# Kernel tuning notes

Measured on AMD Instinct MI355X. Metric: run time of the kernel, lower is better.

The kernel has to match this reference:

```python
import jax, jax.numpy as jnp
import numpy as np

# dims: batch, tokens, model dim, heads, head_dim, context len, n_blocks, ffn dim
B, L, D, H, HD, S, NB, DFF = 1, 3072, 1024, 16, 64, 512, 2, 4096
T3, H3, W3 = 12, 16, 16  # latent video grid, T3*H3*W3 == L


def _ln(x):
    # LayerNorm, elementwise_affine=False, eps=1e-6
    m = jnp.mean(x, axis=-1, keepdims=True)
    v = jnp.mean(jnp.square(x - m), axis=-1, keepdims=True)
    return (x - m) * jax.lax.rsqrt(v + 1e-6)


def _rot_half(x):
    x1, x2 = jnp.split(x, 2, axis=-1)
    return jnp.concatenate([-x2, x1], axis=-1)


def _rope3d(head_dim, t, h, w):
    d = head_dim // 6
    def band(n):
        freqs = 1.0 / 10000.0 ** (np.arange(0, 2 * d, 2, dtype=np.float32) / (2 * d))
        return np.outer(np.arange(n, dtype=np.float32), freqs)  # [n, d]
    te, he, we = band(t), band(h), band(w)
    rope = np.zeros((t, h, w, head_dim), dtype=np.float32)
    rope[:, :, :, :d] = te[:, None, None, :]
    rope[:, :, :, d:2 * d] = he[None, :, None, :]
    rope[:, :, :, 2 * d:3 * d] = we[None, None, :, :]
    return jnp.asarray(rope.reshape(t * h * w, head_dim))


def _forward(x, timestep_emb, context_emb, rope_emb, adaW, adab, sqW, skW, svW,
             soW, sob, cqW, ckW, cvW, coW, cob, f1W, f1b, f2W, f2b):
    Bv, Lv, Dv = x.shape
    hd = rope_emb.shape[-1]
    nh = Dv // hd
    scale = hd ** -0.5
    cos = jnp.cos(rope_emb)[None, None]  # [1,1,L,hd]
    sin = jnp.sin(rope_emb)[None, None]

    def heads(y):  # [B,N,D] -> [B,H,N,hd]
        return y.reshape(Bv, -1, nh, hd).transpose(0, 2, 1, 3)

    def merge(y):  # [B,H,L,hd] -> [B,L,D]
        return y.transpose(0, 2, 1, 3).reshape(Bv, Lv, Dv)

    for i in range(adaW.shape[0]):
        mods = timestep_emb @ adaW[i].T + adab[i]  # [B, 6D]
        sh_msa, sc_msa, g_msa, sh_mlp, sc_mlp, g_mlp = jnp.split(mods, 6, axis=-1)
        # --- AdaLN + self-attention with RoPE ---
        hx = _ln(x) * (1.0 + sc_msa[:, None, :]) + sh_msa[:, None, :]
        q, k, v = heads(hx @ sqW[i].T), heads(hx @ skW[i].T), heads(hx @ svW[i].T)
        q = q * cos + _rot_half(q) * sin
        k = k * cos + _rot_half(k) * sin
        a = jax.nn.softmax(jnp.einsum('bhld,bhmd->bhlm', q, k) * scale, axis=-1)
        o = merge(jnp.einsum('bhlm,bhmd->bhld', a, v))
        x = x + g_msa[:, None, :] * (o @ soW[i].T + sob[i])
        # --- cross-attention (no gate, no modulation) ---
        hx = _ln(x)
        q = heads(hx @ cqW[i].T)
        k = heads(context_emb @ ckW[i].T)
        v = heads(context_emb @ cvW[i].T)
        a = jax.nn.softmax(jnp.einsum('bhld,bhsd->bhls', q, k) * scale, axis=-1)
        o = merge(jnp.einsum('bhls,bhsd->bhld', a, v))
        x = x + (o @ coW[i].T + cob[i])
        # --- AdaLN + MLP (exact GELU) ---
        hx = _ln(x) * (1.0 + sc_mlp[:, None, :]) + sh_mlp[:, None, :]
        hx = jax.nn.gelu(hx @ f1W[i].T + f1b[i], approximate=False)
        x = x + g_mlp[:, None, :] * (hx @ f2W[i].T + f2b[i])
    return x


def setup_inputs() -> dict:
    ks = jax.random.split(jax.random.key(0), 20)
    s = 0.02
    return {
        'x': jax.random.normal(ks[0], (B, L, D), jnp.float32),
        'timestep_emb': jax.random.normal(ks[1], (B, D), jnp.float32),
        'context_emb': jax.random.normal(ks[2], (B, S, D), jnp.float32),
        'rope_emb': _rope3d(HD, T3, H3, W3),
        'adaW': jax.random.normal(ks[3], (NB, 6 * D, D), jnp.float32) * s,
        'adab': jnp.zeros((NB, 6 * D), jnp.float32),
        'sqW': jax.random.normal(ks[4], (NB, D, D), jnp.float32) * s,
        'skW': jax.random.normal(ks[5], (NB, D, D), jnp.float32) * s,
        'svW': jax.random.normal(ks[6], (NB, D, D), jnp.float32) * s,
        'soW': jax.random.normal(ks[7], (NB, D, D), jnp.float32) * s,
        'sob': jnp.zeros((NB, D), jnp.float32),
        'cqW': jax.random.normal(ks[8], (NB, D, D), jnp.float32) * s,
        'ckW': jax.random.normal(ks[9], (NB, D, D), jnp.float32) * s,
        'cvW': jax.random.normal(ks[10], (NB, D, D), jnp.float32) * s,
        'coW': jax.random.normal(ks[11], (NB, D, D), jnp.float32) * s,
        'cob': jnp.zeros((NB, D), jnp.float32),
        'f1W': jax.random.normal(ks[12], (NB, DFF, D), jnp.float32) * s,
        'f1b': jnp.zeros((NB, DFF), jnp.float32),
        'f2W': jax.random.normal(ks[13], (NB, D, DFF), jnp.float32) * s,
        'f2b': jnp.zeros((NB, D), jnp.float32),
    }


def reference(x, timestep_emb, context_emb, rope_emb, adaW, adab, sqW, skW, svW,
              soW, sob, cqW, ckW, cvW, coW, cob, f1W, f1b, f2W, f2b):
    return _forward(x, timestep_emb, context_emb, rope_emb, adaW, adab, sqW, skW,
                    svW, soW, sob, cqW, ckW, cvW, coW, cob, f1W, f1b, f2W, f2b)
```

## Files before the change

### kernel.cpp

```cpp
#include <hip/hip_runtime.h>
#include <math.h>

typedef __attribute__((ext_vector_type(8))) short bf16x8;
typedef __attribute__((ext_vector_type(4))) float f32x4;
typedef unsigned short u16;
typedef unsigned int u32;

#define DEV static __device__ __forceinline__

typedef __attribute__((address_space(3))) u32 lds_u32;
typedef const __attribute__((address_space(1))) u32 glb_u32;

DEV void gload16(const void* g, void* l){
  __builtin_amdgcn_global_load_lds((glb_u32*)g, (lds_u32*)l, 16, 0, 0);
}

DEV u16 f2bf(float f){
  u32 u = __builtin_bit_cast(u32, f);
  u32 r = (u + 0x7fffu + ((u >> 16) & 1u)) >> 16;
  return (u16)r;
}
DEV float bf2f(u16 h){
  u32 u = ((u32)h) << 16;
  return __builtin_bit_cast(float, u);
}
DEV u32 cvtpk(float a, float b){
  u32 r;
  asm("v_cvt_pk_bf16_f32 %0, %1, %2" : "=v"(r) : "v"(a), "v"(b));
  return r;
}
DEV float gelu_exact(float x){ return 0.5f*x*(1.f+erff(x*0.70710678118654752f)); }

#define QSCALE 0.18033688f

DEV void xcd_remap(int &bx, int &by){
  int gx = gridDim.x, gy = gridDim.y;
  int n = gx*gy;
  if ((n & 7) == 0){
    int id = by*gx + bx;
    int q = n >> 3;
    int sid = (id & 7)*q + (id >> 3);
    bx = sid % gx;
    by = sid / gx;
  }
}

__global__ __launch_bounds__(256) void k_copy_f32(const float* __restrict__ in, float* __restrict__ out, int n4){
  int i = blockIdx.x*256 + threadIdx.x;
  if (i < n4) ((float4*)out)[i] = ((const float4*)in)[i];
}

__global__ __launch_bounds__(256) void k_cvt_bf16(const float* __restrict__ in, u16* __restrict__ out, int n4){
  int i = blockIdx.x*256 + threadIdx.x;
  if (i < n4){
    float4 v = ((const float4*)in)[i];
    ushort4 o;
    o.x = f2bf(v.x); o.y = f2bf(v.y); o.z = f2bf(v.z); o.w = f2bf(v.w);
    ((ushort4*)out)[i] = o;
  }
}

struct CvtArgs { const float4* s[16]; ushort4* d[16]; };
__global__ __launch_bounds__(256) void k_cvt_all(CvtArgs a){
  int i = blockIdx.x*256 + threadIdx.x;
  int seg = i >> 19;
  int off = i & 0x7FFFF;
  float4 v = a.s[seg][off];
  ushort4 o;
  o.x = f2bf(v.x); o.y = f2bf(v.y); o.z = f2bf(v.z); o.w = f2bf(v.w);
  a.d[seg][off] = o;
}

__global__ __launch_bounds__(256) void k_trig(const float* __restrict__ rope,
    float2* __restrict__ ctq, float2* __restrict__ ctk){
  int i = blockIdx.x*256 + threadIdx.x;
  int d = i & 63;
  float a = rope[i];
  float c = cosf(a), s = sinf(a);
  float sg = (d < 32) ? -s : s;
  ctk[i] = make_float2(c, sg);
  ctq[i] = make_float2(c*QSCALE, sg*QSCALE);
}

__global__ __launch_bounds__(256) void k_ada(const float* __restrict__ te,
    const float* __restrict__ adaW, const float* __restrict__ adab,
    float* __restrict__ mods){
  int row = blockIdx.x*4 + (threadIdx.x>>6);
  int lane = threadIdx.x & 63;
  const float* wr = adaW + (size_t)row*1024;
  float s = 0.f;
  #pragma unroll
  for (int j=0; j<4; j++){
    int c = lane*4 + j*256;
    float4 a = *(const float4*)(te + c);
    float4 b = *(const float4*)(wr + c);
    s += a.x*b.x + a.y*b.y + a.z*b.z + a.w*b.w;
  }
  #pragma unroll
  for (int off=32; off; off>>=1) s += __shfl_down(s, off);
  if (!lane) mods[row] = s + adab[row];
}

__global__ __launch_bounds__(256) void k_ln_mod(const float* __restrict__ x,
    const float* __restrict__ sh, const float* __restrict__ sc,
    u16* __restrict__ out){
  int row = blockIdx.x, t = threadIdx.x;
  const float* xr = x + (size_t)row*1024;
  float4 v = ((const float4*)xr)[t];
  float s  = v.x+v.y+v.z+v.w;
  float sq = v.x*v.x+v.y*v.y+v.z*v.z+v.w*v.w;
  #pragma unroll
  for (int off=32; off; off>>=1){ s += __shfl_down(s,off); sq += __shfl_down(sq,off); }
  __shared__ float red[8];
  int w = t>>6, lane = t&63;
  if (!lane){ red[w] = s; red[4+w] = sq; }
  __syncthreads();
  s  = red[0]+red[1]+red[2]+red[3];
  sq = red[4]+red[5]+red[6]+red[7];
  float mean = s*(1.f/1024.f);
  float var  = sq*(1.f/1024.f) - mean*mean;
  float rst  = rsqrtf(var + 1e-6f);
  float vv[4] = {v.x, v.y, v.z, v.w};
  ushort4 o;
  u16 ob[4];
  #pragma unroll
  for (int j=0;j<4;j++){
    int col = t*4+j;
    float y = (vv[j]-mean)*rst;
    if (sh) y = y*(1.f + sc[col]) + sh[col];
    ob[j] = f2bf(y);
  }
  o.x=ob[0]; o.y=ob[1]; o.z=ob[2]; o.w=ob[3];
  *(ushort4*)(out + (size_t)row*1024 + t*4) = o;
}

__global__ __launch_bounds__(256) void k_rope(u16* __restrict__ q, u16* __restrict__ k,
    const float* __restrict__ rope){
  int idx = blockIdx.x*256 + threadIdx.x;
  int d = idx & 31;
  int h = (idx >> 5) & 15;
  int p = idx >> 9;
  const float* rr = rope + (size_t)p*64;
  float a0 = rr[d], a1 = rr[d+32];
  float c0 = cosf(a0), s0 = sinf(a0);
  float c1 = cosf(a1), s1 = sinf(a1);
  size_t o = (size_t)p*1024 + h*64 + d;
  float q0 = bf2f(q[o]), q1 = bf2f(q[o+32]);
  q[o]    = f2bf((q0*c0 - q1*s0)*QSCALE);
  q[o+32] = f2bf((q1*c1 + q0*s1)*QSCALE);
  float k0 = bf2f(k[o]), k1 = bf2f(k[o+32]);
  k[o]    = f2bf(k0*c0 - k1*s0);
  k[o+32] = f2bf(k1*c1 + k0*s1);
}

DEV void gemm_loop(const u16* __restrict__ X, const u16* __restrict__ W,
                   int bm, int bn, int ld, int lenK, u16* As, u16* Bs, f32x4 acc[4][4])
{
  int t = threadIdx.x;
  int w = t>>6, lane = t&63;
  int wr = (w>>1)*64, wc = (w&1)*64;
  int fr = lane&15, g = lane>>4;
  int arow = lane>>2, acol = (lane&3)*8;
  const u16* xp = X + (size_t)(bm + w*32 + arow)*ld + acol;
  const u16* wp = W + (size_t)(bn + w*32 + arow)*ld + acol;
  int nk = lenK >> 5;
  {
    u16* a = As + w*1024; u16* b = Bs + w*1024;
    gload16(xp, a);             gload16(xp + (size_t)16*ld, a + 512);
    gload16(wp, b);             gload16(wp + (size_t)16*ld, b + 512);
  }
  for (int kt = 0; kt < nk; ++kt){
    __syncthreads();
    int cur = kt & 1;
    if (kt + 1 < nk){
      int nb = cur ^ 1;
      int k0 = (kt+1) << 5;
      u16* a = As + nb*4096 + w*1024; u16* b = Bs + nb*4096 + w*1024;
      gload16(xp + k0, a);        gload16(xp + k0 + (size_t)16*ld, a + 512);
      gload16(wp + k0, b);        gload16(wp + k0 + (size_t)16*ld, b + 512);
    }
    const u16* ab = As + cur*4096;
    const u16* bb = Bs + cur*4096;
    bf16x8 a[4], b[4];
    #pragma unroll
    for (int i=0;i<4;i++) a[i] = *(const bf16x8*)(ab + (wr+i*16+fr)*32 + g*8);
    #pragma unroll
    for (int i=0;i<4;i++) b[i] = *(const bf16x8*)(bb + (wc+i*16+fr)*32 + g*8);
    __builtin_amdgcn_s_setprio(1);
    #pragma unroll
    for (int i=0;i<4;i++)
      #pragma unroll
      for (int j=0;j<4;j++)
        acc[i][j] = __builtin_amdgcn_mfma_f32_16x16x32_bf16(a[i], b[j], acc[i][j], 0, 0, 0);
    __builtin_amdgcn_s_setprio(0);
  }
}

template<int EPI>
__global__ __launch_bounds__(256) void k_gemm_bf16(
    const u16* __restrict__ X, const u16* __restrict__ W,
    const float* __restrict__ bias,
    u16* __restrict__ Yout,
    const float* __restrict__ resin, float* __restrict__ resout,
    const float* __restrict__ gate,
    int M, int N, int K)
{
  __shared__ __align__(16) u16 As[2*128*32];
  __shared__ __align__(16) u16 Bs[2*128*32];
  int bx = blockIdx.x, by = blockIdx.y;
  xcd_remap(bx, by);
  int bm = bx*128, bn = by*128;
  f32x4 acc[4][4] = {};
  gemm_loop(X, W, bm, bn, K, K, As, Bs, acc);
  int lane = threadIdx.x & 63, w = threadIdx.x>>6;
  int wr = (w>>1)*64, wc = (w&1)*64;
  int fr = lane&15, g = lane>>4;
  #pragma unroll
  for (int i=0;i<4;i++){
    #pragma unroll
    for (int j=0;j<4;j++){
      int col = bn + wc + j*16 + fr;
      float bv = bias ? bias[col] : 0.f;
      #pragma unroll
      for (int r=0;r<4;r++){
        int row = bm + wr + i*16 + g*4 + r;
        float y = acc[i][j][r] + bv;
        if (EPI == 1){
          Yout[(size_t)row*N + col] = f2bf(gelu_exact(y));
        } else if (EPI == 2){
          float gt = gate ? gate[col] : 1.f;
          resout[(size_t)row*N + col] = resin[(size_t)row*N + col] + gt*y;
        } else {
          Yout[(size_t)row*N + col] = f2bf(y*QSCALE);
        }
      }
    }
  }
}

__global__ __launch_bounds__(256) void k_gemm_part(
    const u16* __restrict__ X, const u16* __restrict__ W,
    float* __restrict__ pp, int M, int N, int K, int Ks)
{
  __shared__ __align__(16) u16 As[2*128*32];
  __shared__ __align__(16) u16 Bs[2*128*32];
  int bx = blockIdx.x, by = blockIdx.y;
  xcd_remap(bx, by);
  int s = blockIdx.z;
  int bm = bx*128, bn = by*128;
  f32x4 acc[4][4] = {};
  gemm_loop(X + (size_t)s*Ks, W + (size_t)s*Ks, bm, bn, K, Ks, As, Bs, acc);
  float* out = pp + (size_t)s*M*N;
  int lane = threadIdx.x & 63, w = threadIdx.x>>6;
  int wr = (w>>1)*64, wc = (w&1)*64;
  int fr = lane&15, g = lane>>4;
  #pragma unroll
  for (int i=0;i<4;i++)
    #pragma unroll
    for (int j=0;j<4;j++){
      int col = bn + wc + j*16 + fr;
      #pragma unroll
      for (int r=0;r<4;r++){
        int row = bm + wr + i*16 + g*4 + r;
        out[(size_t)row*N + col] = acc[i][j][r];
      }
    }
}

template<int EPI>
__global__ __launch_bounds__(256) void k_reduce(
    const float* __restrict__ pp, int S, const float* __restrict__ bias,
    const float* __restrict__ resin, float* __restrict__ resout,
    const float* __restrict__ gate, u16* __restrict__ Ybf,
    int MN, int N)
{
  int idx = blockIdx.x*256 + threadIdx.x;
  int base = idx*4;
  if (base >= MN) return;
  float4 s4 = *(const float4*)(pp + base);
  for (int s=1; s<S; ++s){
    float4 t4 = *(const float4*)(pp + (size_t)s*MN + base);
    s4.x += t4.x; s4.y += t4.y; s4.z += t4.z; s4.w += t4.w;
  }
  int col = base & (N-1);
  float b0=0,b1=0,b2=0,b3=0;
  if (bias){ b0=bias[col]; b1=bias[col+1]; b2=bias[col+2]; b3=bias[col+3]; }
  if (EPI == 2){
    float g0=1,g1=1,g2=1,g3=1;
    if (gate){ g0=gate[col]; g1=gate[col+1]; g2=gate[col+2]; g3=gate[col+3]; }
    float4 rv = *(const float4*)(resin + base);
    float4 o;
    o.x = rv.x + g0*(s4.x+b0);
    o.y = rv.y + g1*(s4.y+b1);
    o.z = rv.z + g2*(s4.z+b2);
    o.w = rv.w + g3*(s4.w+b3);
    *(float4*)(resout + base) = o;
  } else {
    ushort4 o;
    o.x = f2bf((s4.x+b0)*QSCALE);
    o.y = f2bf((s4.y+b1)*QSCALE);
    o.z = f2bf((s4.z+b2)*QSCALE);
    o.w = f2bf((s4.w+b3)*QSCALE);
    *(ushort4*)(Ybf + base) = o;
  }
}

template<int MOD>
__global__ __launch_bounds__(256) void k_reduce_ln(
    const float* __restrict__ pp, int S, const float* __restrict__ bias,
    const float* __restrict__ resin, float* __restrict__ resout,
    const float* __restrict__ gate,
    const float* __restrict__ sh, const float* __restrict__ sc,
    u16* __restrict__ hx)
{
  int row = blockIdx.x, t = threadIdx.x;
  size_t base = (size_t)row*1024 + t*4;
  const size_t MN = (size_t)3072*1024;
  float4 s4 = *(const float4*)(pp + base);
  for (int s=1; s<S; ++s){
    float4 t4 = *(const float4*)(pp + (size_t)s*MN + base);
    s4.x += t4.x; s4.y += t4.y; s4.z += t4.z; s4.w += t4.w;
  }
  int col = t*4;
  float b0=0,b1=0,b2=0,b3=0;
  if (bias){ b0=bias[col]; b1=bias[col+1]; b2=bias[col+2]; b3=bias[col+3]; }
  float g0=1,g1=1,g2=1,g3=1;
  if (gate){ g0=gate[col]; g1=gate[col+1]; g2=gate[col+2]; g3=gate[col+3]; }
  float4 rv = *(const float4*)(resin + base);
  float y[4];
  y[0] = rv.x + g0*(s4.x+b0);
  y[1] = rv.y + g1*(s4.y+b1);
  y[2] = rv.z + g2*(s4.z+b2);
  y[3] = rv.w + g3*(s4.w+b3);
  float4 ov; ov.x=y[0]; ov.y=y[1]; ov.z=y[2]; ov.w=y[3];
  *(float4*)(resout + base) = ov;
  float s  = y[0]+y[1]+y[2]+y[3];
  float sq = y[0]*y[0]+y[1]*y[1]+y[2]*y[2]+y[3]*y[3];
  #pragma unroll
  for (int off=32; off; off>>=1){ s += __shfl_down(s,off); sq += __shfl_down(sq,off); }
  __shared__ float red[8];
  int w = t>>6, lane = t&63;
  if (!lane){ red[w] = s; red[4+w] = sq; }
  __syncthreads();
  s  = red[0]+red[1]+red[2]+red[3];
  sq = red[4]+red[5]+red[6]+red[7];
  float mean = s*(1.f/1024.f);
  float var  = sq*(1.f/1024.f) - mean*mean;
  float rst  = rsqrtf(var + 1e-6f);
  ushort4 o;
  u16 ob[4];
  #pragma unroll
  for (int j=0;j<4;j++){
    float yy = (y[j]-mean)*rst;
    if (MOD) yy = yy*(1.f + sc[col+j]) + sh[col+j];
    ob[j] = f2bf(yy);
  }
  o.x=ob[0]; o.y=ob[1]; o.z=ob[2]; o.w=ob[3];
  *(ushort4*)(hx + base) = o;
}

template<int MODE>
__global__ __launch_bounds__(256) void k_qkv(
    const u16* __restrict__ X,
    const u16* __restrict__ W0, const u16* __restrict__ W1, const u16* __restrict__ W2,
    u16* __restrict__ Y0, u16* __restrict__ Y1, u16* __restrict__ VT,
    const float2* __restrict__ ctq, const float2* __restrict__ ctk,
    int M, int ldvt)
{
  __shared__ __align__(16) u16 As[2*128*32];
  __shared__ __align__(16) u16 Bs[2*128*32];
  int bx = blockIdx.x, by = blockIdx.y;
  xcd_remap(bx, by);
  int bm = bx*128, bn = by*128;
  int sel = bn >> 10;
  int bnl = bn & 1023;
  const u16* W = (sel==0 ? W0 : (sel==1 ? W1 : W2));
  f32x4 acc[4][4] = {};
  gemm_loop(X, W, bm, bnl, 1024, 1024, As, Bs, acc);
  int lane = threadIdx.x & 63, w = threadIdx.x>>6;
  int wr = (w>>1)*64, wc = (w&1)*64;
  int fr = lane&15, g = lane>>4;
  if (sel < 2){
    u16* Y = (sel==0) ? Y0 : Y1;
    const float2* ct = (sel==0) ? ctq : ctk;
    #pragma unroll
    for (int i=0;i<4;i++)
      #pragma unroll
      for (int j=0;j<4;j++){
        int col = bnl + wc + j*16 + fr;
        int d = j*16 + fr;
        #pragma unroll
        for (int r=0;r<4;r++){
          int row = bm + wr + i*16 + g*4 + r;
          float2 cs = ct[row*64 + d];
          float yv = acc[i][j][r]*cs.x + acc[i][j^2][r]*cs.y;
          Y[(size_t)row*1024 + col] = f2bf(yv);
        }
      }
  } else {
    #pragma unroll
    for (int i=0;i<4;i++)
      #pragma unroll
      for (int j=0;j<4;j++){
        int col = bnl + wc + j*16 + fr;
        int row0 = bm + wr + i*16 + g*4;
        uint2 pk;
        pk.x = cvtpk(acc[i][j][0], acc[i][j][1]);
        pk.y = cvtpk(acc[i][j][2], acc[i][j][3]);
        *(uint2*)(VT + (size_t)col*ldvt + row0) = pk;
      }
  }
}

__global__ __launch_bounds__(256) void k_kv64(
    const u16* __restrict__ X,
    const u16* __restrict__ Wk, const u16* __restrict__ Wv,
    u16* __restrict__ Kout, u16* __restrict__ VTout, int ldvt)
{
  __shared__ __align__(16) u16 As[2*64*32];
  __shared__ __align__(16) u16 Bs[2*64*32];
  int bx = blockIdx.x, by = blockIdx.y;
  xcd_remap(bx, by);
  int bm = bx*64;
  int sel = by >> 4;
  int bnl = (by & 15)*64;
  const u16* W = sel ? Wv : Wk;
  int t = threadIdx.x, w = t>>6, lane = t&63;
  int wr = (w>>1)*32, wc = (w&1)*32;
  int fr = lane&15, g = lane>>4;
  f32x4 acc[2][2] = {};
  int arow = lane>>2, acol = (lane&3)*8;
  const u16* xp = X + (size_t)(bm + w*16 + arow)*1024 + acol;
  const u16* wp = W + (size_t)(bnl + w*16 + arow)*1024 + acol;
  {
    gload16(xp, As + w*512);
    gload16(wp, Bs + w*512);
  }
  for (int kt = 0; kt < 32; ++kt){
    __syncthreads();
    int cur = kt & 1;
    if (kt + 1 < 32){
      int nb = cur ^ 1;
      int k0 = (kt+1) << 5;
      gload16(xp + k0, As + nb*2048 + w*512);
      gload16(wp + k0, Bs + nb*2048 + w*512);
    }
    const u16* ab = As + cur*2048;
    const u16* bb = Bs + cur*2048;
    bf16x8 a[2], b[2];
    #pragma unroll
    for (int i=0;i<2;i++) a[i] = *(const bf16x8*)(ab + (wr+i*16+fr)*32 + g*8);
    #pragma unroll
    for (int i=0;i<2;i++) b[i] = *(const bf16x8*)(bb + (wc+i*16+fr)*32 + g*8);
    __builtin_amdgcn_s_setprio(1);
    #pragma unroll
    for (int i=0;i<2;i++)
      #pragma unroll
      for (int j=0;j<2;j++)
        acc[i][j] = __builtin_amdgcn_mfma_f32_16x16x32_bf16(a[i], b[j], acc[i][j], 0, 0, 0);
    __builtin_amdgcn_s_setprio(0);
  }
  #pragma unroll
  for (int i=0;i<2;i++)
    #pragma unroll
    for (int j=0;j<2;j++){
      int col = bnl + wc + j*16 + fr;
      if (sel == 0){
        #pragma unroll
        for (int r=0;r<4;r++){
          int row = bm + wr + i*16 + g*4 + r;
          Kout[(size_t)row*1024 + col] = f2bf(acc[i][j][r]);
        }
      } else {
        int row0 = bm + wr + i*16 + g*4;
        uint2 pk;
        pk.x = cvtpk(acc[i][j][0], acc[i][j][1]);
        pk.y = cvtpk(acc[i][j][2], acc[i][j][3]);
        *(uint2*)(VTout + (size_t)col*ldvt + row0) = pk;
      }
    }
}

template<int EPI>
__global__ __launch_bounds__(256) void k_gemm_f32(
    const u16* __restrict__ X, const float* __restrict__ W,
    const float* __restrict__ bias,
    u16* __restrict__ Yout,
    const float* __restrict__ resin, float* __restrict__ resout,
    const float* __restrict__ gate,
    int M, int N, int K)
{
  __shared__ __align__(16) u16 As[128][32];
  __shared__ __align__(16) u16 Bs[128][40];
  int bx = blockIdx.x, by = blockIdx.y;
  xcd_remap(bx, by);
  int bm = bx*128, bn = by*128;
  int t = threadIdx.x;
  int w = t>>6, lane = t&63;
  int wr = (w>>1)*64, wc = (w&1)*64;
  int fr = lane&15, g = lane>>4;
  f32x4 acc[4][4] = {};
  int arow = lane>>2, acol = (lane&3)*8;
  int srow = t>>2, scol = (t&3)*8;
  for (int k0=0; k0<K; k0+=32){
    #pragma unroll
    for (int inst=0; inst<2; ++inst){
      int r = w*32 + inst*16 + arow;
      gload16(X + (size_t)(bm+r)*K + k0 + acol, &As[w*32+inst*16][0]);
    }
    #pragma unroll
    for (int it=0; it<2; ++it){
      const float* wp = W + (size_t)(bn+srow+it*64)*K + k0 + scol;
      float4 f0 = *(const float4*)(wp);
      float4 f1 = *(const float4*)(wp+4);
      uint4 bw;
      bw.x = (u32)f2bf(f0.x) | ((u32)f2bf(f0.y)<<16);
      bw.y = (u32)f2bf(f0.z) | ((u32)f2bf(f0.w)<<16);
      bw.z = (u32)f2bf(f1.x) | ((u32)f2bf(f1.y)<<16);
      bw.w = (u32)f2bf(f1.z) | ((u32)f2bf(f1.w)<<16);
      *(uint4*)&Bs[srow+it*64][scol] = bw;
    }
    __syncthreads();
    bf16x8 a[4], b[4];
    #pragma unroll
    for (int i=0;i<4;i++) a[i] = *(const bf16x8*)&As[wr+i*16+fr][g*8];
    #pragma unroll
    for (int i=0;i<4;i++) b[i] = *(const bf16x8*)&Bs[wc+i*16+fr][g*8];
    #pragma unroll
    for (int i=0;i<4;i++)
      #pragma unroll
      for (int j=0;j<4;j++)
        acc[i][j] = __builtin_amdgcn_mfma_f32_16x16x32_bf16(a[i], b[j], acc[i][j], 0, 0, 0);
    __syncthreads();
  }
  #pragma unroll
  for (int i=0;i<4;i++){
    #pragma unroll
    for (int j=0;j<4;j++){
      int col = bn + wc + j*16 + fr;
      float bv = bias ? bias[col] : 0.f;
      #pragma unroll
      for (int r=0;r<4;r++){
        int row = bm + wr + i*16 + g*4 + r;
        float y = acc[i][j][r] + bv;
        if (EPI == 0){
          Yout[(size_t)row*N + col] = f2bf(y);
        } else if (EPI == 1){
          Yout[(size_t)row*N + col] = f2bf(gelu_exact(y));
        } else if (EPI == 2){
          float gt = gate ? gate[col] : 1.f;
          resout[(size_t)row*N + col] = resin[(size_t)row*N + col] + gt*y;
        } else if (EPI == 3){
          Yout[(size_t)col*M + row] = f2bf(y);
        } else {
          Yout[(size_t)row*N + col] = f2bf(y*QSCALE);
        }
      }
    }
  }
}

__global__ __launch_bounds__(128) void k_flash(
    const u16* __restrict__ Q, const u16* __restrict__ Kb, const u16* __restrict__ VT,
    u16* __restrict__ O, int Lkv)
{
  __shared__ __align__(16) u16 Ks[2*64*64];
  __shared__ __align__(16) u16 Vs[2*64*64];
  __shared__ __align__(16) u16 Ps[2][32][72];
  int bx = blockIdx.x, by = blockIdx.y;
  xcd_remap(bx, by);
  int h = by;
  int q0 = bx*64;
  int t = threadIdx.x, w = t>>6, lane = t&63;
  int fr = lane&15, g = lane>>4;
  bf16x8 aq0[2], aq1[2];
  #pragma unroll
  for (int qg=0; qg<2; ++qg){
    const u16* qrow = Q + (size_t)(q0 + w*32 + qg*16 + fr)*1024 + h*64;
    aq0[qg] = *(const bf16x8*)(qrow + g*8);
    aq1[qg] = *(const bf16x8*)(qrow + 32 + g*8);
  }
  f32x4 accO[2][4] = {};
  float l0 = 0.f, l1 = 0.f;
  int slot = lane & 7, rop = lane >> 3;
  const u16* kbase = Kb + (size_t)h*64;
  const u16* vbase = VT + (size_t)h*64*Lkv;
  int nt = Lkv >> 6;
  auto stage = [&](int tt, int buf){
    int k0 = tt << 6;
    #pragma unroll
    for (int ps=0; ps<4; ++ps){
      int row = ps*16 + w*8 + rop;
      int ss = slot ^ (row & 7);
      gload16(kbase + (size_t)(k0+row)*1024 + ss*8, Ks + buf*4096 + row*64);
      gload16(vbase + (size_t)row*Lkv + k0 + ss*8, Vs + buf*4096 + row*64);
    }
  };
  stage(0, 0);
  for (int tt=0; tt<nt; ++tt){
    __syncthreads();
    int cur = tt & 1;
    if (tt+1 < nt) stage(tt+1, cur^1);
    const u16* kc = Ks + cur*4096;
    const u16* vc = Vs + cur*4096;
    f32x4 st0[4] = {}, st1[4] = {};
    __builtin_amdgcn_s_setprio(1);
    #pragma unroll
    for (int kb=0;kb<4;kb++){
      int rowK = kb*16 + fr;
      bf16x8 kA0 = *(const bf16x8*)(kc + rowK*64 + ((g  ) ^ (rowK&7))*8);
      bf16x8 kA1 = *(const bf16x8*)(kc + rowK*64 + ((4+g) ^ (rowK&7))*8);
      st0[kb] = __builtin_amdgcn_mfma_f32_16x16x32_bf16(kA0, aq0[0], st0[kb], 0,0,0);
      st0[kb] = __builtin_amdgcn_mfma_f32_16x16x32_bf16(kA1, aq1[0], st0[kb], 0,0,0);
      st1[kb] = __builtin_amdgcn_mfma_f32_16x16x32_bf16(kA0, aq0[1], st1[kb], 0,0,0);
      st1[kb] = __builtin_amdgcn_mfma_f32_16x16x32_bf16(kA1, aq1[1], st1[kb], 0,0,0);
    }
    __builtin_amdgcn_s_setprio(0);
    {
      float ts = 0.f;
      u32 pk[8];
      #pragma unroll
      for (int kb=0;kb<4;kb++){
        float p0 = exp2f(st0[kb][0]);
        float p1 = exp2f(st0[kb][1]);
        float p2 = exp2f(st0[kb][2]);
        float p3 = exp2f(st0[kb][3]);
        ts += (p0+p1)+(p2+p3);
        pk[kb*2]   = cvtpk(p0,p1);
        pk[kb*2+1] = cvtpk(p2,p3);
      }
      ts += __shfl_xor(ts, 16);
      ts += __shfl_xor(ts, 32);
      l0 += ts;
      #pragma unroll
      for (int kb=0;kb<4;kb++){
        uint2 pv; pv.x = pk[kb*2]; pv.y = pk[kb*2+1];
        *(uint2*)&Ps[w][fr][kb*16 + g*4] = pv;
      }
    }
    {
      float ts = 0.f;
      u32 pk[8];
      #pragma unroll
      for (int kb=0;kb<4;kb++){
        float p0 = exp2f(st1[kb][0]);
        float p1 = exp2f(st1[kb][1]);
        float p2 = exp2f(st1[kb][2]);
        float p3 = exp2f(st1[kb][3]);
        ts += (p0+p1)+(p2+p3);
        pk[kb*2]   = cvtpk(p0,p1);
        pk[kb*2+1] = cvtpk(p2,p3);
      }
      ts += __shfl_xor(ts, 16);
      ts += __shfl_xor(ts, 32);
      l1 += ts;
      #pragma unroll
      for (int kb=0;kb<4;kb++){
        uint2 pv; pv.x = pk[kb*2]; pv.y = pk[kb*2+1];
        *(uint2*)&Ps[w][16+fr][kb*16 + g*4] = pv;
      }
    }
    bf16x8 ap0g0 = *(const bf16x8*)&Ps[w][fr][g*8];
    bf16x8 ap1g0 = *(const bf16x8*)&Ps[w][fr][32 + g*8];
    bf16x8 ap0g1 = *(const bf16x8*)&Ps[w][16+fr][g*8];
    bf16x8 ap1g1 = *(const bf16x8*)&Ps[w][16+fr][32 + g*8];
    __builtin_amdgcn_s_setprio(1);
    #pragma unroll
    for (int nd=0; nd<4; nd++){
      int rowV = nd*16 + fr;
      bf16x8 vB0 = *(const bf16x8*)(vc + rowV*64 + ((g  ) ^ (rowV&7))*8);
      bf16x8 vB1 = *(const bf16x8*)(vc + rowV*64 + ((4+g) ^ (rowV&7))*8);
      accO[0][nd] = __builtin_amdgcn_mfma_f32_16x16x32_bf16(ap0g0, vB0, accO[0][nd], 0,0,0);
      accO[0][nd] = __builtin_amdgcn_mfma_f32_16x16x32_bf16(ap1g0, vB1, accO[0][nd], 0,0,0);
      accO[1][nd] = __builtin_amdgcn_mfma_f32_16x16x32_bf16(ap0g1, vB0, accO[1][nd], 0,0,0);
      accO[1][nd] = __builtin_amdgcn_mfma_f32_16x16x32_bf16(ap1g1, vB1, accO[1][nd], 0,0,0);
    }
    __builtin_amdgcn_s_setprio(0);
  }
  #pragma unroll
  for (int qg=0; qg<2; ++qg){
    float rl = 1.f / (qg ? l1 : l0);
    #pragma unroll
    for (int r=0;r<4;r++){
      float rlq = __shfl(rl, g*4+r);
      int row = q0 + w*32 + qg*16 + g*4 + r;
      #pragma unroll
      for (int nd=0; nd<4; nd++)
        O[(size_t)row*1024 + h*64 + nd*16 + fr] = f2bf(accO[qg][nd][r] * rlq);
    }
  }
}

extern "C" void kernel_launch(void* const* d_in, const int* in_sizes, int n_in,
                              void* d_out, int out_size, void* d_ws, size_t ws_size,
                              hipStream_t stream){
  const float* x_in = (const float*)d_in[0];
  const float* te   = (const float*)d_in[1];
  const float* ctx  = (const float*)d_in[2];
  const float* rope = (const float*)d_in[3];
  const float* adaW = (const float*)d_in[4];
  const float* adab = (const float*)d_in[5];
  const float* sqW  = (const float*)d_in[6];
  const float* skW  = (const float*)d_in[7];
  const float* svW  = (const float*)d_in[8];
  const float* soW  = (const float*)d_in[9];
  const float* sob  = (const float*)d_in[10];
  const float* cqW  = (const float*)d_in[11];
  const float* ckW  = (const float*)d_in[12];
  const float* cvW  = (const float*)d_in[13];
  const float* coW  = (const float*)d_in[14];
  const float* cob  = (const float*)d_in[15];
  const float* f1W  = (const float*)d_in[16];
  const float* f1b  = (const float*)d_in[17];
  const float* f2W  = (const float*)d_in[18];
  const float* f2b  = (const float*)d_in[19];
  float* x = (float*)d_out;

  char* p = (char*)d_ws;
  size_t used = 0;
  auto alloc = [&](size_t bytes){
    void* r = (void*)(p + used);
    used += (bytes + 255) & ~(size_t)255;
    return r;
  };
  u16* hx   = (u16*)alloc((size_t)3072*1024*2);
  u16* qb   = (u16*)alloc((size_t)3072*1024*2);
  u16* kb   = (u16*)alloc((size_t)3072*1024*2);
  u16* vt   = (u16*)alloc((size_t)1024*3072*2);
  u16* ob   = (u16*)alloc((size_t)3072*1024*2);
  u16* mid  = (u16*)alloc((size_t)3072*4096*2);
  u16* ctxb = (u16*)alloc((size_t)512*1024*2);
  float* mods = (float*)alloc((size_t)2*6144*4);
  float2* ctq = (float2*)alloc((size_t)3072*64*8);
  float2* ctk = (float2*)alloc((size_t)3072*64*8);
  size_t base_used = used;
  const size_t NW_SMALL = (size_t)2*1024*1024;
  const size_t NW_BIG   = (size_t)2*4096*1024;
  size_t wbytes = (8*NW_SMALL + 2*NW_BIG)*2;
  bool pre = (base_used + wbytes + 4096) <= ws_size;

  u16 *sqWb=nullptr,*skWb=nullptr,*svWb=nullptr,*soWb=nullptr,
      *cqWb=nullptr,*ckWb=nullptr,*cvWb=nullptr,*coWb=nullptr,
      *f1Wb=nullptr,*f2Wb=nullptr;
  if (pre){
    sqWb=(u16*)alloc(NW_SMALL*2); skWb=(u16*)alloc(NW_SMALL*2);
    svWb=(u16*)alloc(NW_SMALL*2); soWb=(u16*)alloc(NW_SMALL*2);
    cqWb=(u16*)alloc(NW_SMALL*2); ckWb=(u16*)alloc(NW_SMALL*2);
    cvWb=(u16*)alloc(NW_SMALL*2); coWb=(u16*)alloc(NW_SMALL*2);
    f1Wb=(u16*)alloc(NW_BIG*2);   f2Wb=(u16*)alloc(NW_BIG*2);
  }
  const size_t PPN = (size_t)4*3072*1024;
  float* pp = nullptr;
  bool splitok = pre && (used + PPN*4 + 4096) <= ws_size;
  if (splitok) pp = (float*)alloc(PPN*4);
  const int MN = 3072*1024;

  if (pre){
    CvtArgs ca;
    const float* smallW[8] = {sqW,skW,svW,soW,cqW,ckW,cvW,coW};
    u16* smallD[8] = {sqWb,skWb,svWb,soWb,cqWb,ckWb,cvWb,coWb};
    for (int s=0; s<8; ++s){ ca.s[s] = (const float4*)smallW[s]; ca.d[s] = (ushort4*)smallD[s]; }
    for (int qd=0; qd<4; ++qd){
      ca.s[8+qd]  = (const float4*)f1W + (size_t)qd*524288;
      ca.d[8+qd]  = (ushort4*)f1Wb + (size_t)qd*524288;
      ca.s[12+qd] = (const float4*)f2W + (size_t)qd*524288;
      ca.d[12+qd] = (ushort4*)f2Wb + (size_t)qd*524288;
    }
    k_cvt_all<<<32768, 256, 0, stream>>>(ca);
  }
  k_cvt_bf16<<<512, 256, 0, stream>>>(ctx, ctxb, 131072);
  k_ada<<<3072, 256, 0, stream>>>(te, adaW, adab, mods);
  k_trig<<<768, 256, 0, stream>>>(rope, ctq, ctk);
  if (!splitok) k_copy_f32<<<3072, 256, 0, stream>>>(x_in, x, 786432);

  for (int i=0; i<2; ++i){
    const float* mi  = mods + (size_t)i*6144;
    const float* mi2 = mods + 6144;
    size_t wo = (size_t)i*1024*1024;
    size_t wof = (size_t)i*4096*1024;
    if (i == 0 || !splitok)
      k_ln_mod<<<3072,256,0,stream>>>(i==0 ? x_in : x, mi+0, mi+1024, hx);
    if (pre){
      k_qkv<0><<<dim3(24,24),256,0,stream>>>(hx, sqWb+wo, skWb+wo, svWb+wo, qb, kb, vt, ctq, ctk, 3072, 3072);
    } else {
      k_gemm_f32<0><<<dim3(24,8),256,0,stream>>>(hx, sqW+wo, nullptr, qb, nullptr,nullptr,nullptr, 3072,1024,1024);
      k_gemm_f32<0><<<dim3(24,8),256,0,stream>>>(hx, skW+wo, nullptr, kb, nullptr,nullptr,nullptr, 3072,1024,1024);
      k_gemm_f32<3><<<dim3(24,8),256,0,stream>>>(hx, svW+wo, nullptr, vt, nullptr,nullptr,nullptr, 3072,1024,1024);
      k_rope<<<6144,256,0,stream>>>(qb, kb, rope);
    }
    k_flash<<<dim3(48,16),128,0,stream>>>(qb, kb, vt, ob, 3072);
    if (splitok){
      k_gemm_part<<<dim3(24,8,2),256,0,stream>>>(ob, soWb+wo, pp, 3072,1024,1024,512);
      k_reduce_ln<0><<<3072,256,0,stream>>>(pp, 2, sob+(size_t)i*1024,
          (i==0 ? x_in : (const float*)x), x, mi+2048, nullptr, nullptr, hx);
    } else if (pre){
      k_gemm_bf16<2><<<dim3(24,8),256,0,stream>>>(ob, soWb+wo, sob+(size_t)i*1024, nullptr, x, x, mi+2048, 3072,1024,1024);
      k_ln_mod<<<3072,256,0,stream>>>(x, nullptr, nullptr, hx);
    } else {
      k_gemm_f32<2><<<dim3(24,8),256,0,stream>>>(ob, soW+wo, sob+(size_t)i*1024, nullptr, x, x, mi+2048, 3072,1024,1024);
      k_ln_mod<<<3072,256,0,stream>>>(x, nullptr, nullptr, hx);
    }
    if (splitok){
      k_gemm_part<<<dim3(24,8,2),256,0,stream>>>(hx, cqWb+wo, pp, 3072,1024,1024,512);
      k_reduce<4><<<3072,256,0,stream>>>(pp, 2, nullptr, nullptr, nullptr, nullptr, qb, MN, 1024);
      k_kv64<<<dim3(8,32),256,0,stream>>>(ctxb, ckWb+wo, cvWb+wo, kb, vt, 512);
    } else if (pre){
      k_gemm_bf16<4><<<dim3(24,8),256,0,stream>>>(hx, cqWb+wo, nullptr, qb, nullptr,nullptr,nullptr, 3072,1024,1024);
      k_kv64<<<dim3(8,32),256,0,stream>>>(ctxb, ckWb+wo, cvWb+wo, kb, vt, 512);
    } else {
      k_gemm_f32<4><<<dim3(24,8),256,0,stream>>>(hx, cqW+wo, nullptr, qb, nullptr,nullptr,nullptr, 3072,1024,1024);
      k_gemm_f32<0><<<dim3(4,8),256,0,stream>>>(ctxb, ckW+wo, nullptr, kb, nullptr,nullptr,nullptr, 512,1024,1024);
      k_gemm_f32<3><<<dim3(4,8),256,0,stream>>>(ctxb, cvW+wo, nullptr, vt, nullptr,nullptr,nullptr, 512,1024,1024);
    }
    k_flash<<<dim3(48,16),128,0,stream>>>(qb, kb, vt, ob, 512);
    if (splitok){
      k_gemm_part<<<dim3(24,8,2),256,0,stream>>>(ob, coWb+wo, pp, 3072,1024,1024,512);
      k_reduce_ln<1><<<3072,256,0,stream>>>(pp, 2, cob+(size_t)i*1024, x, x, nullptr, mi+3072, mi+4096, hx);
    } else if (pre){
      k_gemm_bf16<2><<<dim3(24,8),256,0,stream>>>(ob, coWb+wo, cob+(size_t)i*1024, nullptr, x, x, nullptr, 3072,1024,1024);
      k_ln_mod<<<3072,256,0,stream>>>(x, mi+3072, mi+4096, hx);
    } else {
      k_gemm_f32<2><<<dim3(24,8),256,0,stream>>>(ob, coW+wo, cob+(size_t)i*1024, nullptr, x, x, nullptr, 3072,1024,1024);
      k_ln_mod<<<3072,256,0,stream>>>(x, mi+3072, mi+4096, hx);
    }
    if (pre){
      k_gemm_bf16<1><<<dim3(24,32),256,0,stream>>>(hx, f1Wb+wof, f1b+(size_t)i*4096, mid, nullptr,nullptr,nullptr, 3072,4096,1024);
    } else {
      k_gemm_f32<1><<<dim3(24,32),256,0,stream>>>(hx, f1W+wof, f1b+(size_t)i*4096, mid, nullptr,nullptr,nullptr, 3072,4096,1024);
    }
    if (splitok){
      k_gemm_part<<<dim3(24,8,4),256,0,stream>>>(mid, f2Wb+wof, pp, 3072,1024,4096,1024);
      if (i == 0)
        k_reduce_ln<1><<<3072,256,0,stream>>>(pp, 4, f2b, x, x, mi+5120, mi2+0, mi2+1024, hx);
      else
        k_reduce<2><<<3072,256,0,stream>>>(pp, 4, f2b+1024, x, x, mi+5120, nullptr, MN, 1024);
    } else if (pre){
      k_gemm_bf16<2><<<dim3(24,8),256,0,stream>>>(mid, f2Wb+wof, f2b+(size_t)i*1024, nullptr, x, x, mi+5120, 3072,1024,4096);
    } else {
      k_gemm_f32<2><<<dim3(24,8),256,0,stream>>>(mid, f2W+wof, f2b+(size_t)i*1024, nullptr, x, x, mi+5120, 3072,1024,4096);
    }
  }
}
```

Before: 816.0 us.

## Restructure flash attention to four waves with software-pipelined PV matmul

The flash kernel moves from 2 waves handling 32 query rows each to 4 waves handling 16 rows each, which doubles threads per block and halves per-wave register state. The P·V MFMA for tile t-1 is deferred and issued alongside the QK^T MFMAs of tile t. V fragments are kept in registers across iterations so the softmax exp work can overlap with matrix work. The cost is extra registers for the carried V fragments, and K/V tiles are no longer shared across as many query rows per wave.

```diff
diff --git a/kernel.cpp b/kernel.cpp
--- a/kernel.cpp
+++ b/kernel.cpp
@@ -560,134 +560,117 @@
   }
 }
 
-__global__ __launch_bounds__(128) void k_flash(
+__global__ __launch_bounds__(256) void k_flash(
     const u16* __restrict__ Q, const u16* __restrict__ Kb, const u16* __restrict__ VT,
     u16* __restrict__ O, int Lkv)
 {
   __shared__ __align__(16) u16 Ks[2*64*64];
   __shared__ __align__(16) u16 Vs[2*64*64];
-  __shared__ __align__(16) u16 Ps[2][32][72];
+  __shared__ __align__(16) u16 Ps[4][16][72];
   int bx = blockIdx.x, by = blockIdx.y;
   xcd_remap(bx, by);
   int h = by;
   int q0 = bx*64;
   int t = threadIdx.x, w = t>>6, lane = t&63;
   int fr = lane&15, g = lane>>4;
-  bf16x8 aq0[2], aq1[2];
-  #pragma unroll
-  for (int qg=0; qg<2; ++qg){
-    const u16* qrow = Q + (size_t)(q0 + w*32 + qg*16 + fr)*1024 + h*64;
-    aq0[qg] = *(const bf16x8*)(qrow + g*8);
-    aq1[qg] = *(const bf16x8*)(qrow + 32 + g*8);
-  }
-  f32x4 accO[2][4] = {};
-  float l0 = 0.f, l1 = 0.f;
+  const u16* qrow = Q + (size_t)(q0 + w*16 + fr)*1024 + h*64;
+  bf16x8 aq0 = *(const bf16x8*)(qrow + g*8);
+  bf16x8 aq1 = *(const bf16x8*)(qrow + 32 + g*8);
+  f32x4 accO[4] = {};
+  float l = 0.f;
   int slot = lane & 7, rop = lane >> 3;
   const u16* kbase = Kb + (size_t)h*64;
   const u16* vbase = VT + (size_t)h*64*Lkv;
   int nt = Lkv >> 6;
-  auto stage = [&](int tt, int buf){
+  auto stage = [&](int tt){
+    int buf = tt & 1;
     int k0 = tt << 6;
     #pragma unroll
-    for (int ps=0; ps<4; ++ps){
-      int row = ps*16 + w*8 + rop;
+    for (int inst=0; inst<2; ++inst){
+      int row = w*16 + inst*8 + rop;
       int ss = slot ^ (row & 7);
       gload16(kbase + (size_t)(k0+row)*1024 + ss*8, Ks + buf*4096 + row*64);
       gload16(vbase + (size_t)row*Lkv + k0 + ss*8, Vs + buf*4096 + row*64);
     }
   };
-  stage(0, 0);
+  stage(0);
+  bf16x8 vp0[4], vp1[4];
   for (int tt=0; tt<nt; ++tt){
     __syncthreads();
     int cur = tt & 1;
-    if (tt+1 < nt) stage(tt+1, cur^1);
     const u16* kc = Ks + cur*4096;
     const u16* vc = Vs + cur*4096;
-    f32x4 st0[4] = {}, st1[4] = {};
+    bf16x8 vn0[4], vn1[4];
+    #pragma unroll
+    for (int nd=0; nd<4; nd++){
+      int rowV = nd*16 + fr;
+      vn0[nd] = *(const bf16x8*)(vc + rowV*64 + ((g  ) ^ (rowV&7))*8);
+      vn1[nd] = *(const bf16x8*)(vc + rowV*64 + ((4+g) ^ (rowV&7))*8);
+    }
+    bf16x8 ap0, ap1;
+    if (tt > 0){
+      ap0 = *(const bf16x8*)&Ps[w][fr][g*8];
+      ap1 = *(const bf16x8*)&Ps[w][fr][32 + g*8];
+    }
+    if (tt+1 < nt) stage(tt+1);
+    f32x4 st[4] = {};
     __builtin_amdgcn_s_setprio(1);
     #pragma unroll
     for (int kb=0;kb<4;kb++){
       int rowK = kb*16 + fr;
-      bf16x8 kA0 = *(const bf16x8*)(kc + rowK*64 + ((g  ) ^ (rowK&7))*8);
-      bf16x8 kA1 = *(const bf16x8*)(kc + rowK*64 + ((4+g) ^ (rowK&7))*8);
-      st0[kb] = __builtin_amdgcn_mfma_f32_16x16x32_bf16(kA0, aq0[0], st0[kb], 0,0,0);
-      st0[kb] = __builtin_amdgcn_mfma_f32_16x16x32_bf16(kA1, aq1[0], st0[kb], 0,0,0);
-      st1[kb] = __builtin_amdgcn_mfma_f32_16x16x32_bf16(kA0, aq0[1], st1[kb], 0,0,0);
-      st1[kb] = __builtin_amdgcn_mfma_f32_16x16x32_bf16(kA1, aq1[1], st1[kb], 0,0,0);
+      bf16x8 b0 = *(const bf16x8*)(kc + rowK*64 + ((g  ) ^ (rowK&7))*8);
+      bf16x8 b1 = *(const bf16x8*)(kc + rowK*64 + ((4+g) ^ (rowK&7))*8);
+      st[kb] = __builtin_amdgcn_mfma_f32_16x16x32_bf16(b0, aq0, st[kb], 0,0,0);
+      st[kb] = __builtin_amdgcn_mfma_f32_16x16x32_bf16(b1, aq1, st[kb], 0,0,0);
+    }
+    if (tt > 0){
+      #pragma unroll
+      for (int nd=0; nd<4; nd++){
+        accO[nd] = __builtin_amdgcn_mfma_f32_16x16x32_bf16(ap0, vp0[nd], accO[nd], 0,0,0);
+        accO[nd] = __builtin_amdgcn_mfma_f32_16x16x32_bf16(ap1, vp1[nd], accO[nd], 0,0,0);
+      }
     }
     __builtin_amdgcn_s_setprio(0);
-    {
-      float ts = 0.f;
-      u32 pk[8];
-      #pragma unroll
-      for (int kb=0;kb<4;kb++){
-        float p0 = exp2f(st0[kb][0]);
-        float p1 = exp2f(st0[kb][1]);
-        float p2 = exp2f(st0[kb][2]);
-        float p3 = exp2f(st0[kb][3]);
-        ts += (p0+p1)+(p2+p3);
-        pk[kb*2]   = cvtpk(p0,p1);
-        pk[kb*2+1] = cvtpk(p2,p3);
-      }
-      ts += __shfl_xor(ts, 16);
-      ts += __shfl_xor(ts, 32);
-      l0 += ts;
-      #pragma unroll
-      for (int kb=0;kb<4;kb++){
-        uint2 pv; pv.x = pk[kb*2]; pv.y = pk[kb*2+1];
-        *(uint2*)&Ps[w][fr][kb*16 + g*4] = pv;
-      }
-    }
-    {
-      float ts = 0.f;
-      u32 pk[8];
-      #pragma unroll
-      for (int kb=0;kb<4;kb++){
-        float p0 = exp2f(st1[kb][0]);
-        float p1 = exp2f(st1[kb][1]);
-        float p2 = exp2f(st1[kb][2]);
-        float p3 = exp2f(st1[kb][3]);
-        ts += (p0+p1)+(p2+p3);
-        pk[kb*2]   = cvtpk(p0,p1);
-        pk[kb*2+1] = cvtpk(p2,p3);
-      }
-      ts += __shfl_xor(ts, 16);
-      ts += __shfl_xor(ts, 32);
-      l1 += ts;
-      #pragma unroll
-      for (int kb=0;kb<4;kb++){
-        uint2 pv; pv.x = pk[kb*2]; pv.y = pk[kb*2+1];
-        *(uint2*)&Ps[w][16+fr][kb*16 + g*4] = pv;
-      }
-    }
-    bf16x8 ap0g0 = *(const bf16x8*)&Ps[w][fr][g*8];
-    bf16x8 ap1g0 = *(const bf16x8*)&Ps[w][fr][32 + g*8];
-    bf16x8 ap0g1 = *(const bf16x8*)&Ps[w][16+fr][g*8];
-    bf16x8 ap1g1 = *(const bf16x8*)&Ps[w][16+fr][32 + g*8];
-    __builtin_amdgcn_s_setprio(1);
+    float ts = 0.f;
+    u32 pk[8];
+    #pragma unroll
+    for (int kb=0;kb<4;kb++){
+      float p0 = exp2f(st[kb][0]);
+      float p1 = exp2f(st[kb][1]);
+      float p2 = exp2f(st[kb][2]);
+      float p3 = exp2f(st[kb][3]);
+      ts += (p0+p1)+(p2+p3);
+      pk[kb*2]   = cvtpk(p0,p1);
+      pk[kb*2+1] = cvtpk(p2,p3);
+    }
+    ts += __shfl_xor(ts, 16);
+    ts += __shfl_xor(ts, 32);
+    l += ts;
+    #pragma unroll
+    for (int kb=0;kb<4;kb++){
+      uint2 pv; pv.x = pk[kb*2]; pv.y = pk[kb*2+1];
+      *(uint2*)&Ps[w][fr][kb*16 + g*4] = pv;
+    }
+    #pragma unroll
+    for (int nd=0; nd<4; nd++){ vp0[nd] = vn0[nd]; vp1[nd] = vn1[nd]; }
+  }
+  {
+    bf16x8 ap0 = *(const bf16x8*)&Ps[w][fr][g*8];
+    bf16x8 ap1 = *(const bf16x8*)&Ps[w][fr][32 + g*8];
     #pragma unroll
     for (int nd=0; nd<4; nd++){
-      int rowV = nd*16 + fr;
-      bf16x8 vB0 = *(const bf16x8*)(vc + rowV*64 + ((g  ) ^ (rowV&7))*8);
-      bf16x8 vB1 = *(const bf16x8*)(vc + rowV*64 + ((4+g) ^ (rowV&7))*8);
-      accO[0][nd] = __builtin_amdgcn_mfma_f32_16x16x32_bf16(ap0g0, vB0, accO[0][nd], 0,0,0);
-      accO[0][nd] = __builtin_amdgcn_mfma_f32_16x16x32_bf16(ap1g0, vB1, accO[0][nd], 0,0,0);
-      accO[1][nd] = __builtin_amdgcn_mfma_f32_16x16x32_bf16(ap0g1, vB0, accO[1][nd], 0,0,0);
-      accO[1][nd] = __builtin_amdgcn_mfma_f32_16x16x32_bf16(ap1g1, vB1, accO[1][nd], 0,0,0);
-    }
-    __builtin_amdgcn_s_setprio(0);
-  }
-  #pragma unroll
-  for (int qg=0; qg<2; ++qg){
-    float rl = 1.f / (qg ? l1 : l0);
-    #pragma unroll
-    for (int r=0;r<4;r++){
-      float rlq = __shfl(rl, g*4+r);
-      int row = q0 + w*32 + qg*16 + g*4 + r;
-      #pragma unroll
-      for (int nd=0; nd<4; nd++)
-        O[(size_t)row*1024 + h*64 + nd*16 + fr] = f2bf(accO[qg][nd][r] * rlq);
-    }
+      accO[nd] = __builtin_amdgcn_mfma_f32_16x16x32_bf16(ap0, vp0[nd], accO[nd], 0,0,0);
+      accO[nd] = __builtin_amdgcn_mfma_f32_16x16x32_bf16(ap1, vp1[nd], accO[nd], 0,0,0);
+    }
+  }
+  float rl = 1.f / l;
+  #pragma unroll
+  for (int r=0;r<4;r++){
+    float rlq = __shfl(rl, g*4+r);
+    int row = q0 + w*16 + g*4 + r;
+    #pragma unroll
+    for (int nd=0; nd<4; nd++)
+      O[(size_t)row*1024 + h*64 + nd*16 + fr] = f2bf(accO[nd][r] * rlq);
   }
 }
 
@@ -788,7 +771,7 @@
       k_gemm_f32<3><<<dim3(24,8),256,0,stream>>>(hx, svW+wo, nullptr, vt, nullptr,nullptr,nullptr, 3072,1024,1024);
       k_rope<<<6144,256,0,stream>>>(qb, kb, rope);
     }
-    k_flash<<<dim3(48,16),128,0,stream>>>(qb, kb, vt, ob, 3072);
+    k_flash<<<dim3(48,16),256,0,stream>>>(qb, kb, vt, ob, 3072);
     if (splitok){
       k_gemm_part<<<dim3(24,8,2),256,0,stream>>>(ob, soWb+wo, pp, 3072,1024,1024,512);
       k_reduce_ln<0><<<3072,256,0,stream>>>(pp, 2, sob+(size_t)i*1024,
@@ -812,7 +795,7 @@
       k_gemm_f32<0><<<dim3(4,8),256,0,stream>>>(ctxb, ckW+wo, nullptr, kb, nullptr,nullptr,nullptr, 512,1024,1024);
       k_gemm_f32<3><<<dim3(4,8),256,0,stream>>>(ctxb, cvW+wo, nullptr, vt, nullptr,nullptr,nullptr, 512,1024,1024);
     }
-    k_flash<<<dim3(48,16),128,0,stream>>>(qb, kb, vt, ob, 512);
+    k_flash<<<dim3(48,16),256,0,stream>>>(qb, kb, vt, ob, 512);
     if (splitok){
       k_gemm_part<<<dim3(24,8,2),256,0,stream>>>(ob, coWb+wo, pp, 3072,1024,1024,512);
       k_reduce_ln<1><<<3072,256,0,stream>>>(pp, 2, cob+(size_t)i*1024, x, x, nullptr, mi+3072, mi+4096, hx);
```

Result: faster. 788.8 us (-3.3%).
